# Optimization experiments

Hardware: AMD Instinct MI355X
Metric: run time of the kernel (lower is better)

## Reference

```python
import jax, jax.numpy as jnp
import numpy as np

CUTOFF = 1.5  # matches init cutoff
BIG = 1e6    # stand-in for masked-out (diagonal) distances


def _energy(positions, cell, sigma_matrix, epsilon_matrix, alpha_matrix, species):
    n = positions.shape[0]
    # pairwise displacements dr[i, j] = pos[j] - pos[i], minimum image under PBC
    dr = positions[None, :, :] - positions[:, None, :]          # [N, N, 3]
    inv_cell = jnp.linalg.inv(cell)
    frac = dr @ inv_cell
    frac = frac - jnp.round(frac)                               # minimum image
    dr = frac @ cell
    r2 = jnp.sum(dr * dr, axis=-1)                              # [N, N]
    eye = jnp.eye(n, dtype=bool)
    r = jnp.sqrt(jnp.where(eye, 1.0, r2))                       # safe sqrt on diag
    r = jnp.where(eye, BIG, r)                                  # mask self-pairs
    # species-pair parameter gather: [N, N]
    si, sj = species[:, None], species[None, :]
    sig = sigma_matrix[si, sj]
    eps = epsilon_matrix[si, sj]
    alp = alpha_matrix[si, sj]
    within = (r < CUTOFF) & (~eye)
    # soft-sphere pair energy: eps/alpha * (1 - r/sigma)^alpha for r < sigma
    f = jnp.maximum(1.0 - r / sig, 0.0)
    e = (eps / alp) * jnp.power(f, alp)
    e = jnp.where(within, e, 0.0)
    return jnp.sum(e) / 2.0


def setup_inputs() -> dict:
    key = jax.random.key(0)
    k1, k2, k3, k4, k5 = jax.random.split(key, 5)
    N, S = 4096, 8
    density = 0.8
    L = float((N / density) ** (1.0 / 3.0))
    positions = jax.random.uniform(k1, (N, 3), dtype=jnp.float32) * L
    cell = (L * jnp.eye(3)).astype(jnp.float32)
    species = jax.random.randint(k2, (N,), 0, S)

    def sym(k, base, scale):
        a = jax.random.uniform(k, (S, S), dtype=jnp.float32)
        a = 0.5 * (a + a.T)
        return base + scale * a

    sigma_matrix = sym(k3, 0.9, 0.2)    # ~1.0
    epsilon_matrix = sym(k4, 0.9, 0.2)  # ~1.0
    alpha_matrix = sym(k5, 2.0, 0.5)    # ~2.0-2.5
    return {
        "positions": positions,
        "cell": cell,
        "sigma_matrix": sigma_matrix,
        "epsilon_matrix": epsilon_matrix,
        "alpha_matrix": alpha_matrix,
        "species": species,
    }


def reference(positions, cell, sigma_matrix, epsilon_matrix, alpha_matrix, species):
    energy, g = jax.value_and_grad(
        lambda p: _energy(p, cell, sigma_matrix, epsilon_matrix, alpha_matrix, species)
    )(positions)
    forces = -g
    return energy, forces
```

## Files before the change

### kernel.cpp

```cpp
#include <hip/hip_runtime.h>


#define TI 256
#define TJ 128
#define CUT2 2.25f

__global__ __launch_bounds__(TI) void soft_sphere_kernel(
    const float* __restrict__ pos,
    const float* __restrict__ cell,
    const float* __restrict__ sigm,
    const float* __restrict__ epsm,
    const float* __restrict__ alpm,
    const int*   __restrict__ spec,
    float* __restrict__ out,
    int n)
{
    __shared__ float sh_px[TJ], sh_py[TJ], sh_pz[TJ];
    __shared__ int   sh_sp[TJ];
    __shared__ float sh_sig[64], sh_eps[64], sh_alp[64];
    __shared__ float sh_e[TI / 64];

    const int tid = threadIdx.x;

    if (tid < 64) {
        sh_sig[tid] = sigm[tid];
        sh_eps[tid] = epsm[tid];
        sh_alp[tid] = alpm[tid];
    }

    const int j0 = blockIdx.y * TJ;
    for (int t = tid; t < TJ; t += TI) {
        int j = j0 + t;
        sh_px[t] = pos[3 * j + 0];
        sh_py[t] = pos[3 * j + 1];
        sh_pz[t] = pos[3 * j + 2];
        sh_sp[t] = spec[j];
    }

    const float m00 = cell[0], m01 = cell[1], m02 = cell[2];
    const float m10 = cell[3], m11 = cell[4], m12 = cell[5];
    const float m20 = cell[6], m21 = cell[7], m22 = cell[8];
    const float det = m00 * (m11 * m22 - m12 * m21)
                    - m01 * (m10 * m22 - m12 * m20)
                    + m02 * (m10 * m21 - m11 * m20);
    const float rdet = 1.0f / det;
    const float i00 = (m11 * m22 - m12 * m21) * rdet;
    const float i01 = (m02 * m21 - m01 * m22) * rdet;
    const float i02 = (m01 * m12 - m02 * m11) * rdet;
    const float i10 = (m12 * m20 - m10 * m22) * rdet;
    const float i11 = (m00 * m22 - m02 * m20) * rdet;
    const float i12 = (m02 * m10 - m00 * m12) * rdet;
    const float i20 = (m10 * m21 - m11 * m20) * rdet;
    const float i21 = (m01 * m20 - m00 * m21) * rdet;
    const float i22 = (m00 * m11 - m01 * m10) * rdet;

    const int i = blockIdx.x * TI + tid;
    const float px = pos[3 * i + 0];
    const float py = pos[3 * i + 1];
    const float pz = pos[3 * i + 2];
    const int   si8 = spec[i] << 3;

    __syncthreads();

    float e_acc = 0.0f, fxa = 0.0f, fya = 0.0f, fza = 0.0f;

#pragma unroll 4
    for (int t = 0; t < TJ; ++t) {
        float dx = sh_px[t] - px;
        float dy = sh_py[t] - py;
        float dz = sh_pz[t] - pz;
        float fx = dx * i00 + dy * i10 + dz * i20;
        float fy = dx * i01 + dy * i11 + dz * i21;
        float fz = dx * i02 + dy * i12 + dz * i22;
        fx -= rintf(fx);
        fy -= rintf(fy);
        fz -= rintf(fz);
        float ddx = fx * m00 + fy * m10 + fz * m20;
        float ddy = fx * m01 + fy * m11 + fz * m21;
        float ddz = fx * m02 + fy * m12 + fz * m22;
        float r2 = ddx * ddx + ddy * ddy + ddz * ddz;

        if (r2 < CUT2 && (j0 + t) != i) {
            float r  = sqrtf(r2);
            int  idx = si8 + sh_sp[t];
            float sg = sh_sig[idx];
            float f  = 1.0f - r / sg;
            if (f > 0.0f) {
                float ep  = sh_eps[idx];
                float al  = sh_alp[idx];
                float fa1 = powf(f, al - 1.0f);
                e_acc += ep / al * fa1 * f;
                float c = ep * fa1 / (sg * r);
                fxa -= c * ddx;
                fya -= c * ddy;
                fza -= c * ddz;
            }
        }
    }

    atomicAdd(&out[1 + 3 * i + 0], fxa);
    atomicAdd(&out[1 + 3 * i + 1], fya);
    atomicAdd(&out[1 + 3 * i + 2], fza);

    for (int off = 32; off > 0; off >>= 1)
        e_acc += __shfl_down(e_acc, off, 64);
    if ((tid & 63) == 0) sh_e[tid >> 6] = e_acc;
    __syncthreads();
    if (tid == 0) {
        float tot = 0.0f;
        for (int w = 0; w < TI / 64; ++w) tot += sh_e[w];
        atomicAdd(&out[0], 0.5f * tot);
    }
}

extern "C" void kernel_launch(void* const* d_in, const int* in_sizes, int n_in,
                              void* d_out, int out_size, void* d_ws, size_t ws_size,
                              hipStream_t stream) {
    const float* pos  = (const float*)d_in[0];
    const float* cell = (const float*)d_in[1];
    const float* sigm = (const float*)d_in[2];
    const float* epsm = (const float*)d_in[3];
    const float* alpm = (const float*)d_in[4];
    const int*   spec = (const int*)d_in[5];
    float* out = (float*)d_out;
    const int n = in_sizes[5];

    hipMemsetAsync(out, 0, (size_t)out_size * sizeof(float), stream);

    dim3 grid(n / TI, (n + TJ - 1) / TJ);
    soft_sphere_kernel<<<grid, TI, 0, stream>>>(pos, cell, sigm, epsm, alpm,
                                                spec, out, n);
}
```

Baseline: 97.50 us.

## Add orthorhombic fast path, packed shared tables, fast pow, and smaller j-tile

Adds a runtime branch for diagonal cells that wraps each axis with one scale, rint and FMA, replacing the two 3x3 matrix transforms. Per-species-pair parameters are precomputed into a float4 table (1/sigma, alpha-1, eps/alpha, eps/sigma), and positions plus species are packed into float4 shared entries. powf becomes exp2(e*log2 f) via AMDGCN intrinsics, and division and sqrt become rsqrt. TJ is halved to 64, which doubles the grid and the number of per-atom force atomics. The fast pow drops the accuracy guarantees of powf.

```diff
diff --git a/kernel.cpp b/kernel.cpp
--- a/kernel.cpp
+++ b/kernel.cpp
@@ -2,8 +2,12 @@
 
 
 #define TI 256
-#define TJ 128
+#define TJ 64
 #define CUT2 2.25f
+
+__device__ __forceinline__ float fast_pow(float f, float e) {
+    return __builtin_amdgcn_exp2f(e * __builtin_amdgcn_logf(f));
+}
 
 __global__ __launch_bounds__(TI) void soft_sphere_kernel(
     const float* __restrict__ pos,
@@ -15,85 +19,104 @@
     float* __restrict__ out,
     int n)
 {
-    __shared__ float sh_px[TJ], sh_py[TJ], sh_pz[TJ];
-    __shared__ int   sh_sp[TJ];
-    __shared__ float sh_sig[64], sh_eps[64], sh_alp[64];
-    __shared__ float sh_e[TI / 64];
+    __shared__ float4 sh_pos[TJ];
+    __shared__ float4 sh_tab[64];
+    __shared__ float  sh_e[TI / 64];
 
     const int tid = threadIdx.x;
+    const int j0  = blockIdx.y * TJ;
 
     if (tid < 64) {
-        sh_sig[tid] = sigm[tid];
-        sh_eps[tid] = epsm[tid];
-        sh_alp[tid] = alpm[tid];
-    }
-
-    const int j0 = blockIdx.y * TJ;
-    for (int t = tid; t < TJ; t += TI) {
-        int j = j0 + t;
-        sh_px[t] = pos[3 * j + 0];
-        sh_py[t] = pos[3 * j + 1];
-        sh_pz[t] = pos[3 * j + 2];
-        sh_sp[t] = spec[j];
+        float sg = sigm[tid], ep = epsm[tid], al = alpm[tid];
+        float inv_sg = 1.0f / sg;
+        sh_tab[tid] = make_float4(inv_sg, al - 1.0f, ep / al, ep * inv_sg);
+        int j = j0 + tid;
+        sh_pos[tid] = make_float4(pos[3 * j + 0], pos[3 * j + 1],
+                                  pos[3 * j + 2], __int_as_float(spec[j]));
     }
 
     const float m00 = cell[0], m01 = cell[1], m02 = cell[2];
     const float m10 = cell[3], m11 = cell[4], m12 = cell[5];
     const float m20 = cell[6], m21 = cell[7], m22 = cell[8];
-    const float det = m00 * (m11 * m22 - m12 * m21)
-                    - m01 * (m10 * m22 - m12 * m20)
-                    + m02 * (m10 * m21 - m11 * m20);
-    const float rdet = 1.0f / det;
-    const float i00 = (m11 * m22 - m12 * m21) * rdet;
-    const float i01 = (m02 * m21 - m01 * m22) * rdet;
-    const float i02 = (m01 * m12 - m02 * m11) * rdet;
-    const float i10 = (m12 * m20 - m10 * m22) * rdet;
-    const float i11 = (m00 * m22 - m02 * m20) * rdet;
-    const float i12 = (m02 * m10 - m00 * m12) * rdet;
-    const float i20 = (m10 * m21 - m11 * m20) * rdet;
-    const float i21 = (m01 * m20 - m00 * m21) * rdet;
-    const float i22 = (m00 * m11 - m01 * m10) * rdet;
+    const bool diag = (m01 == 0.0f) & (m02 == 0.0f) & (m10 == 0.0f) &
+                      (m12 == 0.0f) & (m20 == 0.0f) & (m21 == 0.0f);
 
-    const int i = blockIdx.x * TI + tid;
-    const float px = pos[3 * i + 0];
-    const float py = pos[3 * i + 1];
-    const float pz = pos[3 * i + 2];
+    const int   i   = blockIdx.x * TI + tid;
+    const float px  = pos[3 * i + 0];
+    const float py  = pos[3 * i + 1];
+    const float pz  = pos[3 * i + 2];
     const int   si8 = spec[i] << 3;
 
     __syncthreads();
 
     float e_acc = 0.0f, fxa = 0.0f, fya = 0.0f, fza = 0.0f;
 
+    if (diag) {
+        const float iLx = 1.0f / m00, iLy = 1.0f / m11, iLz = 1.0f / m22;
 #pragma unroll 4
-    for (int t = 0; t < TJ; ++t) {
-        float dx = sh_px[t] - px;
-        float dy = sh_py[t] - py;
-        float dz = sh_pz[t] - pz;
-        float fx = dx * i00 + dy * i10 + dz * i20;
-        float fy = dx * i01 + dy * i11 + dz * i21;
-        float fz = dx * i02 + dy * i12 + dz * i22;
-        fx -= rintf(fx);
-        fy -= rintf(fy);
-        fz -= rintf(fz);
-        float ddx = fx * m00 + fy * m10 + fz * m20;
-        float ddy = fx * m01 + fy * m11 + fz * m21;
-        float ddz = fx * m02 + fy * m12 + fz * m22;
-        float r2 = ddx * ddx + ddy * ddy + ddz * ddz;
-
-        if (r2 < CUT2 && (j0 + t) != i) {
-            float r  = sqrtf(r2);
-            int  idx = si8 + sh_sp[t];
-            float sg = sh_sig[idx];
-            float f  = 1.0f - r / sg;
-            if (f > 0.0f) {
-                float ep  = sh_eps[idx];
-                float al  = sh_alp[idx];
-                float fa1 = powf(f, al - 1.0f);
-                e_acc += ep / al * fa1 * f;
-                float c = ep * fa1 / (sg * r);
-                fxa -= c * ddx;
-                fya -= c * ddy;
-                fza -= c * ddz;
+        for (int t = 0; t < TJ; ++t) {
+            float4 pj = sh_pos[t];
+            float dx = pj.x - px;
+            float dy = pj.y - py;
+            float dz = pj.z - pz;
+            dx = fmaf(-rintf(dx * iLx), m00, dx);
+            dy = fmaf(-rintf(dy * iLy), m11, dy);
+            dz = fmaf(-rintf(dz * iLz), m22, dz);
+            float r2 = fmaf(dx, dx, fmaf(dy, dy, dz * dz));
+            if (r2 < CUT2 && (j0 + t) != i) {
+                float4 tab = sh_tab[si8 + __float_as_int(pj.w)];
+                float rinv = rsqrtf(r2);
+                float r    = r2 * rinv;
+                float f    = fmaf(-r, tab.x, 1.0f);
+                if (f > 0.0f) {
+                    float p = fast_pow(f, tab.y);
+                    e_acc = fmaf(tab.z * p, f, e_acc);
+                    float c = tab.w * p * rinv;
+                    fxa = fmaf(-c, dx, fxa);
+                    fya = fmaf(-c, dy, fya);
+                    fza = fmaf(-c, dz, fza);
+                }
+            }
+        }
+    } else {
+        const float det = m00 * (m11 * m22 - m12 * m21)
+                        - m01 * (m10 * m22 - m12 * m20)
+                        + m02 * (m10 * m21 - m11 * m20);
+        const float rdet = 1.0f / det;
+        const float i00 = (m11 * m22 - m12 * m21) * rdet;
+        const float i01 = (m02 * m21 - m01 * m22) * rdet;
+        const float i02 = (m01 * m12 - m02 * m11) * rdet;
+        const float i10 = (m12 * m20 - m10 * m22) * rdet;
+        const float i11 = (m00 * m22 - m02 * m20) * rdet;
+        const float i12 = (m02 * m10 - m00 * m12) * rdet;
+        const float i20 = (m10 * m21 - m11 * m20) * rdet;
+        const float i21 = (m01 * m20 - m00 * m21) * rdet;
+        const float i22 = (m00 * m11 - m01 * m10) * rdet;
+#pragma unroll 2
+        for (int t = 0; t < TJ; ++t) {
+            float4 pj = sh_pos[t];
+            float dx = pj.x - px, dy = pj.y - py, dz = pj.z - pz;
+            float fx = dx * i00 + dy * i10 + dz * i20;
+            float fy = dx * i01 + dy * i11 + dz * i21;
+            float fz = dx * i02 + dy * i12 + dz * i22;
+            fx -= rintf(fx); fy -= rintf(fy); fz -= rintf(fz);
+            float ddx = fx * m00 + fy * m10 + fz * m20;
+            float ddy = fx * m01 + fy * m11 + fz * m21;
+            float ddz = fx * m02 + fy * m12 + fz * m22;
+            float r2 = fmaf(ddx, ddx, fmaf(ddy, ddy, ddz * ddz));
+            if (r2 < CUT2 && (j0 + t) != i) {
+                float4 tab = sh_tab[si8 + __float_as_int(pj.w)];
+                float rinv = rsqrtf(r2);
+                float r    = r2 * rinv;
+                float f    = fmaf(-r, tab.x, 1.0f);
+                if (f > 0.0f) {
+                    float p = fast_pow(f, tab.y);
+                    e_acc = fmaf(tab.z * p, f, e_acc);
+                    float c = tab.w * p * rinv;
+                    fxa = fmaf(-c, ddx, fxa);
+                    fya = fmaf(-c, ddy, fya);
+                    fza = fmaf(-c, ddz, fza);
+                }
             }
         }
     }
@@ -125,7 +148,7 @@
     float* out = (float*)d_out;
     const int n = in_sizes[5];
 
-    hipMemsetAsync(out, 0, (size_t)out_size * sizeof(float), stream);
+    (void)hipMemsetAsync(out, 0, (size_t)out_size * sizeof(float), stream);
 
     dim3 grid(n / TI, (n + TJ - 1) / TJ);
     soft_sphere_kernel<<<grid, TI, 0, stream>>>(pos, cell, sigm, epsm, alpm,
```

Measured after the change: 92.72 us. 1.05x faster.
